# Performance work log

Measured on AMD Instinct MI355X. Metric: run time of the kernel, lower is better.

Reference implementation:

```python
import jax, jax.numpy as jnp
import numpy as np

# config constants
B, T, C = 2, 2048, 1024
N_HEAD = 16
N_FULL = 8           # n_head - int(n_head * ratio_heads)
N_RED = 8            # int(n_head * 0.5)
HEAD_DIM = 64        # C // N_HEAD
RED_DIM = 32         # int(HEAD_DIM * 0.5)
WIN_FULL = 1024      # context_full
WIN_RED = 256        # context_reduced


def setup_inputs() -> dict:
    key = jax.random.key(0)
    ks = jax.random.split(key, 5)
    def w(k, shape, fan_in):
        return jax.random.normal(k, shape, jnp.float32) * (1.0 / np.sqrt(fan_in))
    return {
        "x": jax.random.normal(ks[0], (B, T, C), jnp.float32),
        "w_qkv_full": w(ks[1], (C, 3 * N_FULL * HEAD_DIM), C),
        "w_qk_red": w(ks[2], (C, 2 * N_RED * RED_DIM), C),
        "w_v_red": w(ks[3], (C, N_RED * HEAD_DIM), C),
        "w_proj": w(ks[4], (C, C), C),
    }


def _windowed_attn(q, k, v, window):
    # q,k: [B,H,T,dq], v: [B,H,T,dv]; causal sliding window: 0 <= i-j < window
    d = q.shape[-1]
    scores = jnp.einsum("bhqd,bhkd->bhqk", q, k) / jnp.sqrt(jnp.float32(d))
    i = jnp.arange(q.shape[2])[:, None]
    j = jnp.arange(k.shape[2])[None, :]
    mask = (i - j < 0) | (i - j >= window)
    scores = jnp.where(mask, -jnp.inf, scores)
    p = jax.nn.softmax(scores, axis=-1)
    return jnp.einsum("bhqk,bhkd->bhqd", p, v)


def reference(x, w_qkv_full, w_qk_red, w_v_red, w_proj):
    Bx, Tx, Cx = x.shape
    split_heads = lambda t, d: t.reshape(Bx, Tx, -1, d).transpose(0, 2, 1, 3)

    # full-dim heads
    q, k, v = jnp.split(x @ w_qkv_full, 3, axis=-1)
    y_full = _windowed_attn(split_heads(q, HEAD_DIM), split_heads(k, HEAD_DIM),
                            split_heads(v, HEAD_DIM), WIN_FULL)

    # reduced q/k dim heads (values keep full head_dim)
    qr, kr = jnp.split(x @ w_qk_red, 2, axis=-1)
    vr = x @ w_v_red
    y_red = _windowed_attn(split_heads(qr, RED_DIM), split_heads(kr, RED_DIM),
                           split_heads(vr, HEAD_DIM), WIN_RED)

    y = jnp.concatenate([y_full, y_red], axis=1)          # [B, n_head, T, head_dim]
    y = y.transpose(0, 2, 1, 3).reshape(Bx, Tx, Cx)
    return y @ w_proj
```

## Files before the change

### kernel.cpp

```cpp
#include <hip/hip_runtime.h>
#include <hip/hip_bf16.h>
#include <stdint.h>

#define TT 2048
#define BB 2
#define CC 1024
#define NEGF (-1e30f)

typedef short bf16x8 __attribute__((ext_vector_type(8)));
typedef short bf16x4 __attribute__((ext_vector_type(4)));
typedef float f32x4 __attribute__((ext_vector_type(4)));

__device__ __forceinline__ f32x4 mfma16(bf16x8 a, bf16x8 b, f32x4 c) {
  return __builtin_amdgcn_mfma_f32_16x16x32_bf16(a, b, c, 0, 0, 0);
}

__device__ __forceinline__ uint16_t f2bf(float f) {
  union { float f; uint32_t u; } v; v.f = f;
  uint32_t u = v.u;
  return (uint16_t)((u + 0x7FFFu + ((u >> 16) & 1u)) >> 16);
}

typedef __attribute__((address_space(3))) uint32_t lds_u32;
typedef const __attribute__((address_space(1))) uint32_t glb_u32;
__device__ __forceinline__ void gload_lds16(const uint16_t* g, uint16_t* l) {
  __builtin_amdgcn_global_load_lds((glb_u32*)g, (lds_u32*)l, 16, 0, 0);
}

__global__ __launch_bounds__(256) void k_convert(const float* __restrict__ in,
                                                 uint16_t* __restrict__ out, int n4) {
  int i = blockIdx.x * blockDim.x + threadIdx.x;
  if (i >= n4) return;
  float4 f = ((const float4*)in)[i];
  ushort4 o;
  o.x = f2bf(f.x); o.y = f2bf(f.y); o.z = f2bf(f.z); o.w = f2bf(f.w);
  ((ushort4*)out)[i] = o;
}

__global__ __launch_bounds__(256) void k_transpose(const float* __restrict__ W,
                                                   uint16_t* __restrict__ Wt,
                                                   int K, int N) {
  __shared__ float tile[32][33];
  int tx = threadIdx.x & 31, ty = threadIdx.x >> 5;
  int n0 = blockIdx.x * 32, k0 = blockIdx.y * 32;
#pragma unroll
  for (int r = 0; r < 4; r++)
    tile[ty + r * 8][tx] = W[(size_t)(k0 + ty + r * 8) * N + n0 + tx];
  __syncthreads();
#pragma unroll
  for (int r = 0; r < 4; r++)
    Wt[(size_t)(n0 + ty + r * 8) * K + k0 + tx] = f2bf(tile[tx][ty + r * 8]);
}

template <bool F32OUT>
__global__ __launch_bounds__(256) void k_gemm128(const uint16_t* __restrict__ A,
                                                 const uint16_t* __restrict__ Bt,
                                                 void* __restrict__ Cp,
                                                 int K, int ldc) {
  __shared__ __align__(16) uint16_t Alds[128 * 32];
  __shared__ __align__(16) uint16_t Blds[128 * 32];
  const int tid = threadIdx.x;
  const int lane = tid & 63, wave = tid >> 6;
  const int lr = lane & 15, lg = lane >> 4;
  const int wm = wave & 1, wn = wave >> 1;
  const int m0 = blockIdx.y * 128;
  const int n0 = blockIdx.x * 128;

  f32x4 acc[4][4] = {};

  const int srow = wave * 16 + (lane >> 2);
  const int scol = (lane & 3) * 8;
  const uint16_t* pa_l = A + (size_t)(m0 + srow) * K + scol;
  const uint16_t* pb_l = Bt + (size_t)(n0 + srow) * K + scol;
  uint16_t* alds_w0 = &Alds[(wave * 64) * 8];
  uint16_t* alds_w1 = &Alds[(256 + wave * 64) * 8];
  uint16_t* blds_w0 = &Blds[(wave * 64) * 8];
  uint16_t* blds_w1 = &Blds[(256 + wave * 64) * 8];

  for (int k0 = 0; k0 < K; k0 += 32) {
    __syncthreads();
    gload_lds16(pa_l + k0, alds_w0);
    gload_lds16(pa_l + (size_t)64 * K + k0, alds_w1);
    gload_lds16(pb_l + k0, blds_w0);
    gload_lds16(pb_l + (size_t)64 * K + k0, blds_w1);
    __syncthreads();

    bf16x8 af[4], bfr[4];
#pragma unroll
    for (int mi = 0; mi < 4; mi++)
      af[mi] = *(const bf16x8*)&Alds[(wm * 64 + mi * 16 + lr) * 32 + lg * 8];
#pragma unroll
    for (int ni = 0; ni < 4; ni++)
      bfr[ni] = *(const bf16x8*)&Blds[(wn * 64 + ni * 16 + lr) * 32 + lg * 8];
#pragma unroll
    for (int mi = 0; mi < 4; mi++)
#pragma unroll
      for (int ni = 0; ni < 4; ni++)
        acc[mi][ni] = mfma16(af[mi], bfr[ni], acc[mi][ni]);
  }

#pragma unroll
  for (int mi = 0; mi < 4; mi++)
#pragma unroll
    for (int ni = 0; ni < 4; ni++)
#pragma unroll
      for (int r = 0; r < 4; r++) {
        size_t idx = (size_t)(m0 + wm * 64 + mi * 16 + lg * 4 + r) * ldc
                   + n0 + wn * 64 + ni * 16 + lr;
        if (F32OUT) ((float*)Cp)[idx] = acc[mi][ni][r];
        else        ((uint16_t*)Cp)[idx] = f2bf(acc[mi][ni][r]);
      }
}

__global__ __launch_bounds__(256) void k_vtrans(const uint16_t* __restrict__ QKV,
                                                uint16_t* __restrict__ Vt) {
  __shared__ uint16_t tile[64][72];
  int t0 = blockIdx.x * 64;
  int h = blockIdx.y, b = blockIdx.z;
  int vOff = (h < 8) ? (1024 + h * 64) : (2048 + (h - 8) * 64);
  const uint16_t* src = QKV + ((size_t)b * TT + t0) * 2560 + vOff;
  int tx = threadIdx.x & 15, ty = threadIdx.x >> 4;
#pragma unroll
  for (int p = 0; p < 4; p++)
    *(ushort4*)&tile[ty + p * 16][tx * 4] =
        *(const ushort4*)(src + (size_t)(ty + p * 16) * 2560 + tx * 4);
  __syncthreads();
  uint16_t* dst = Vt + ((size_t)(b * 16 + h) * 64) * TT + t0;
#pragma unroll
  for (int p = 0; p < 4; p++) {
    int dv = ty + p * 16;
    ushort4 o;
    o.x = tile[tx * 4 + 0][dv];
    o.y = tile[tx * 4 + 1][dv];
    o.z = tile[tx * 4 + 2][dv];
    o.w = tile[tx * 4 + 3][dv];
    *(ushort4*)(dst + (size_t)dv * TT + tx * 4) = o;
  }
}

__global__ __launch_bounds__(256) void k_attn(const uint16_t* __restrict__ QKV,
                                              const uint16_t* __restrict__ Vt,
                                              uint16_t* __restrict__ Y) {
  __shared__ __align__(16) uint16_t Klds[64 * 64];
  __shared__ __align__(16) uint16_t Vlds[64 * 64];
  __shared__ __align__(16) uint16_t Plds[4][16][72];
  const int tid = threadIdx.x;
  const int lane = tid & 63, wave = tid >> 6;
  const int lr = lane & 15, lg = lane >> 4;
  const int qt = blockIdx.x & 31;
  const int h = (blockIdx.x >> 5) & 15;
  const int b = blockIdx.x >> 9;
  const int q0b = qt * 64;
  const int q0 = q0b + wave * 16;

  int dqk, window, qOff, kOff;
  if (h < 8) { dqk = 64; window = 1024; qOff = h * 64; kOff = 512 + h * 64; }
  else { int hr = h - 8; dqk = 32; window = 256; qOff = 1536 + hr * 32; kOff = 1792 + hr * 32; }
  const float scale = (dqk == 64) ? 0.125f : 0.17677669529663687f;
  const uint16_t* base = QKV + (size_t)b * TT * 2560;
  const uint16_t* vt = Vt + ((size_t)(b * 16 + h) * 64) * TT;
  const int nf = dqk >> 5;

  bf16x8 qf[2];
  for (int s = 0; s < nf; s++)
    qf[s] = *(const bf16x8*)(base + (size_t)(q0 + lr) * 2560 + qOff + s * 32 + lg * 8);

  float m = NEGF, lsum = 0.f;
  f32x4 o[4] = {};

  int klo_b = q0b - window + 1; if (klo_b < 0) klo_b = 0; klo_b &= ~63;
  const int klo_w = (q0 - window + 1 < 0) ? 0 : (q0 - window + 1);
  const int khi_w = q0 + 15;
  const int q = q0 + lr;

  for (int k0 = klo_b; k0 <= q0b + 63; k0 += 64) {
    __syncthreads();
    if (nf == 2) {
#pragma unroll
      for (int j = 0; j < 2; j++) {
        int c = j * 256 + tid;
        int row = c >> 3, cl = c & 7, sc = cl ^ (row & 7);
        gload_lds16(base + (size_t)(k0 + row) * 2560 + kOff + sc * 8,
                    &Klds[(j * 256 + wave * 64) * 8]);
      }
    } else {
      int row = tid >> 2, cl = tid & 3, sc = cl ^ (row & 3);
      gload_lds16(base + (size_t)(k0 + row) * 2560 + kOff + sc * 8,
                  &Klds[(wave * 64) * 8]);
    }
#pragma unroll
    for (int j = 0; j < 2; j++) {
      int c = j * 256 + tid;
      int row = c >> 3, cl = c & 7, sc = cl ^ (row & 7);
      gload_lds16(vt + (size_t)row * TT + k0 + sc * 8,
                  &Vlds[(j * 256 + wave * 64) * 8]);
    }
    __syncthreads();

    if (k0 > khi_w || k0 + 63 < klo_w) continue;

    f32x4 st[4];
#pragma unroll
    for (int hh = 0; hh < 4; hh++) {
      f32x4 acc = {0.f, 0.f, 0.f, 0.f};
      int row = hh * 16 + lr;
      if (nf == 2) {
        acc = mfma16(*(const bf16x8*)&Klds[row * 64 + ((lg) ^ (row & 7)) * 8], qf[0], acc);
        acc = mfma16(*(const bf16x8*)&Klds[row * 64 + ((4 + lg) ^ (row & 7)) * 8], qf[1], acc);
      } else {
        acc = mfma16(*(const bf16x8*)&Klds[row * 32 + ((lg) ^ (row & 3)) * 8], qf[0], acc);
      }
      st[hh] = acc;
    }
    float tmax = NEGF;
    const bool interior = (k0 + 63 <= q0) && (q0 + 15 - k0 < window);
    if (interior) {
#pragma unroll
      for (int hh = 0; hh < 4; hh++)
#pragma unroll
        for (int r = 0; r < 4; r++) {
          float sv = st[hh][r] * scale;
          st[hh][r] = sv;
          tmax = fmaxf(tmax, sv);
        }
    } else {
#pragma unroll
      for (int hh = 0; hh < 4; hh++)
#pragma unroll
        for (int r = 0; r < 4; r++) {
          int key = k0 + 16 * hh + lg * 4 + r;
          bool ok = (key <= q) && (q - key < window);
          float sv = ok ? st[hh][r] * scale : NEGF;
          st[hh][r] = sv;
          tmax = fmaxf(tmax, sv);
        }
    }
    tmax = fmaxf(tmax, __shfl_xor(tmax, 16));
    tmax = fmaxf(tmax, __shfl_xor(tmax, 32));
    if (!__all(tmax <= m)) {
      float mn = fmaxf(m, tmax);
      float alpha = __expf(m - mn);
      lsum *= alpha;
#pragma unroll
      for (int d = 0; d < 4; d++) o[d] *= alpha;
      m = mn;
    }
    float psum = 0.f;
#pragma unroll
    for (int hh = 0; hh < 4; hh++) {
      bf16x4 pk;
#pragma unroll
      for (int r = 0; r < 4; r++) {
        float sv = st[hh][r];
        float p = (sv > -0.5e30f) ? __expf(sv - m) : 0.f;
        psum += p;
        pk[r] = (short)f2bf(p);
      }
      *(bf16x4*)&Plds[wave][lr][16 * hh + lg * 4] = pk;
    }
    psum += __shfl_xor(psum, 16);
    psum += __shfl_xor(psum, 32);
    lsum += psum;

#pragma unroll
    for (int ks = 0; ks < 2; ks++) {
      bf16x8 pf = *(const bf16x8*)&Plds[wave][lr][ks * 32 + lg * 8];
#pragma unroll
      for (int db = 0; db < 4; db++) {
        int row = db * 16 + lr;
        bf16x8 vf = *(const bf16x8*)&Vlds[row * 64 + ((4 * ks + lg) ^ (row & 7)) * 8];
        o[db] = mfma16(vf, pf, o[db]);
      }
    }
  }
  const float inv = 1.0f / lsum;
  uint16_t* yp = Y + ((size_t)b * TT + q0 + lr) * CC + h * 64;
#pragma unroll
  for (int db = 0; db < 4; db++)
#pragma unroll
    for (int r = 0; r < 4; r++)
      yp[db * 16 + lg * 4 + r] = f2bf(o[db][r] * inv);
}

extern "C" void kernel_launch(void* const* d_in, const int* in_sizes, int n_in,
                              void* d_out, int out_size, void* d_ws, size_t ws_size,
                              hipStream_t stream) {
  const float* x    = (const float*)d_in[0];
  const float* wqkv = (const float*)d_in[1];
  const float* wqk  = (const float*)d_in[2];
  const float* wv   = (const float*)d_in[3];
  const float* wp   = (const float*)d_in[4];

  uint16_t* ws  = (uint16_t*)d_ws;
  uint16_t* xb  = ws;
  uint16_t* WtA = xb  + (size_t)4096 * 1024;
  uint16_t* WtP = WtA + (size_t)2560 * 1024;
  uint16_t* QKV = WtP + (size_t)1024 * 1024;
  uint16_t* Yb  = QKV + (size_t)4096 * 2560;
  uint16_t* Vt  = xb;

  k_convert<<<4096, 256, 0, stream>>>(x, xb, 4096 * 1024 / 4);
  k_transpose<<<dim3(48, 32), 256, 0, stream>>>(wqkv, WtA, 1024, 1536);
  k_transpose<<<dim3(16, 32), 256, 0, stream>>>(wqk, WtA + (size_t)1536 * 1024, 1024, 512);
  k_transpose<<<dim3(16, 32), 256, 0, stream>>>(wv,  WtA + (size_t)2048 * 1024, 1024, 512);
  k_transpose<<<dim3(32, 32), 256, 0, stream>>>(wp,  WtP, 1024, 1024);
  k_gemm128<false><<<dim3(20, 32), 256, 0, stream>>>(xb, WtA, QKV, 1024, 2560);
  k_vtrans<<<dim3(32, 16, 2), 256, 0, stream>>>(QKV, Vt);
  k_attn<<<1024, 256, 0, stream>>>(QKV, Vt, Yb);
  k_gemm128<true><<<dim3(8, 32), 256, 0, stream>>>(Yb, WtP, (float*)d_out, 1024, 1024);
}
```

Measured before the change: 203.9 us.

## Double-buffer K/V LDS tiles in attention to overlap loads with compute

The attention kernel now keeps two LDS buffers for K and V and issues the async global-to-LDS loads for the next key tile before computing on the current one. This replaces the two barriers per iteration with a single vmcnt wait plus barrier at the end. It also raises wave priority around the MFMA sections. The goal is to hide global load latency behind the QK and PV matmuls, at the cost of doubling K/V LDS use, which may lower occupancy.

After: 204.6 us. Within noise of the previous version (+0.4%).

```diff
diff --git a/kernel.cpp b/kernel.cpp
--- a/kernel.cpp
+++ b/kernel.cpp
@@ -141,8 +141,8 @@
 __global__ __launch_bounds__(256) void k_attn(const uint16_t* __restrict__ QKV,
                                               const uint16_t* __restrict__ Vt,
                                               uint16_t* __restrict__ Y) {
-  __shared__ __align__(16) uint16_t Klds[64 * 64];
-  __shared__ __align__(16) uint16_t Vlds[64 * 64];
+  __shared__ __align__(16) uint16_t Klds[2][64 * 64];
+  __shared__ __align__(16) uint16_t Vlds[2][64 * 64];
   __shared__ __align__(16) uint16_t Plds[4][16][72];
   const int tid = threadIdx.x;
   const int lane = tid & 63, wave = tid >> 6;
@@ -172,106 +172,126 @@
   const int klo_w = (q0 - window + 1 < 0) ? 0 : (q0 - window + 1);
   const int khi_w = q0 + 15;
   const int q = q0 + lr;
-
-  for (int k0 = klo_b; k0 <= q0b + 63; k0 += 64) {
-    __syncthreads();
+  const int kend = q0b + 63;
+
+  auto stage = [&](int k0, int buf) {
     if (nf == 2) {
 #pragma unroll
       for (int j = 0; j < 2; j++) {
         int c = j * 256 + tid;
         int row = c >> 3, cl = c & 7, sc = cl ^ (row & 7);
         gload_lds16(base + (size_t)(k0 + row) * 2560 + kOff + sc * 8,
-                    &Klds[(j * 256 + wave * 64) * 8]);
+                    &Klds[buf][(j * 256 + wave * 64) * 8]);
       }
     } else {
       int row = tid >> 2, cl = tid & 3, sc = cl ^ (row & 3);
       gload_lds16(base + (size_t)(k0 + row) * 2560 + kOff + sc * 8,
-                  &Klds[(wave * 64) * 8]);
+                  &Klds[buf][(wave * 64) * 8]);
     }
 #pragma unroll
     for (int j = 0; j < 2; j++) {
       int c = j * 256 + tid;
       int row = c >> 3, cl = c & 7, sc = cl ^ (row & 7);
       gload_lds16(vt + (size_t)row * TT + k0 + sc * 8,
-                  &Vlds[(j * 256 + wave * 64) * 8]);
+                  &Vlds[buf][(j * 256 + wave * 64) * 8]);
     }
-    __syncthreads();
-
-    if (k0 > khi_w || k0 + 63 < klo_w) continue;
-
-    f32x4 st[4];
-#pragma unroll
-    for (int hh = 0; hh < 4; hh++) {
-      f32x4 acc = {0.f, 0.f, 0.f, 0.f};
-      int row = hh * 16 + lr;
-      if (nf == 2) {
-        acc = mfma16(*(const bf16x8*)&Klds[row * 64 + ((lg) ^ (row & 7)) * 8], qf[0], acc);
-        acc = mfma16(*(const bf16x8*)&Klds[row * 64 + ((4 + lg) ^ (row & 7)) * 8], qf[1], acc);
+  };
+
+  stage(klo_b, 0);
+  asm volatile("s_waitcnt vmcnt(0)" ::: "memory");
+  __builtin_amdgcn_s_barrier();
+  __builtin_amdgcn_sched_barrier(0);
+
+  int cur = 0;
+  for (int k0 = klo_b; k0 <= kend; k0 += 64) {
+    const int nxt = k0 + 64;
+    if (nxt <= kend) stage(nxt, cur ^ 1);
+
+    if (!(k0 > khi_w || k0 + 63 < klo_w)) {
+      f32x4 st[4];
+      __builtin_amdgcn_s_setprio(1);
+#pragma unroll
+      for (int hh = 0; hh < 4; hh++) {
+        f32x4 acc = {0.f, 0.f, 0.f, 0.f};
+        int row = hh * 16 + lr;
+        if (nf == 2) {
+          acc = mfma16(*(const bf16x8*)&Klds[cur][row * 64 + ((lg) ^ (row & 7)) * 8], qf[0], acc);
+          acc = mfma16(*(const bf16x8*)&Klds[cur][row * 64 + ((4 + lg) ^ (row & 7)) * 8], qf[1], acc);
+        } else {
+          acc = mfma16(*(const bf16x8*)&Klds[cur][row * 32 + ((lg) ^ (row & 3)) * 8], qf[0], acc);
+        }
+        st[hh] = acc;
+      }
+      __builtin_amdgcn_s_setprio(0);
+      float tmax = NEGF;
+      const bool interior = (k0 + 63 <= q0) && (q0 + 15 - k0 < window);
+      if (interior) {
+#pragma unroll
+        for (int hh = 0; hh < 4; hh++)
+#pragma unroll
+          for (int r = 0; r < 4; r++) {
+            float sv = st[hh][r] * scale;
+            st[hh][r] = sv;
+            tmax = fmaxf(tmax, sv);
+          }
       } else {
-        acc = mfma16(*(const bf16x8*)&Klds[row * 32 + ((lg) ^ (row & 3)) * 8], qf[0], acc);
-      }
-      st[hh] = acc;
+#pragma unroll
+        for (int hh = 0; hh < 4; hh++)
+#pragma unroll
+          for (int r = 0; r < 4; r++) {
+            int key = k0 + 16 * hh + lg * 4 + r;
+            bool ok = (key <= q) && (q - key < window);
+            float sv = ok ? st[hh][r] * scale : NEGF;
+            st[hh][r] = sv;
+            tmax = fmaxf(tmax, sv);
+          }
+      }
+      tmax = fmaxf(tmax, __shfl_xor(tmax, 16));
+      tmax = fmaxf(tmax, __shfl_xor(tmax, 32));
+      if (!__all(tmax <= m)) {
+        float mn = fmaxf(m, tmax);
+        float alpha = __expf(m - mn);
+        lsum *= alpha;
+#pragma unroll
+        for (int d = 0; d < 4; d++) o[d] *= alpha;
+        m = mn;
+      }
+      float psum = 0.f;
+#pragma unroll
+      for (int hh = 0; hh < 4; hh++) {
+        bf16x4 pk;
+#pragma unroll
+        for (int r = 0; r < 4; r++) {
+          float sv = st[hh][r];
+          float p = (sv > -0.5e30f) ? __expf(sv - m) : 0.f;
+          psum += p;
+          pk[r] = (short)f2bf(p);
+        }
+        *(bf16x4*)&Plds[wave][lr][16 * hh + lg * 4] = pk;
+      }
+      psum += __shfl_xor(psum, 16);
+      psum += __shfl_xor(psum, 32);
+      lsum += psum;
+
+      __builtin_amdgcn_s_setprio(1);
+#pragma unroll
+      for (int ks = 0; ks < 2; ks++) {
+        bf16x8 pf = *(const bf16x8*)&Plds[wave][lr][ks * 32 + lg * 8];
+#pragma unroll
+        for (int db = 0; db < 4; db++) {
+          int row = db * 16 + lr;
+          bf16x8 vf = *(const bf16x8*)&Vlds[cur][row * 64 + ((4 * ks + lg) ^ (row & 7)) * 8];
+          o[db] = mfma16(vf, pf, o[db]);
+        }
+      }
+      __builtin_amdgcn_s_setprio(0);
     }
-    float tmax = NEGF;
-    const bool interior = (k0 + 63 <= q0) && (q0 + 15 - k0 < window);
-    if (interior) {
-#pragma unroll
-      for (int hh = 0; hh < 4; hh++)
-#pragma unroll
-        for (int r = 0; r < 4; r++) {
-          float sv = st[hh][r] * scale;
-          st[hh][r] = sv;
-          tmax = fmaxf(tmax, sv);
-        }
-    } else {
-#pragma unroll
-      for (int hh = 0; hh < 4; hh++)
-#pragma unroll
-        for (int r = 0; r < 4; r++) {
-          int key = k0 + 16 * hh + lg * 4 + r;
-          bool ok = (key <= q) && (q - key < window);
-          float sv = ok ? st[hh][r] * scale : NEGF;
-          st[hh][r] = sv;
-          tmax = fmaxf(tmax, sv);
-        }
-    }
-    tmax = fmaxf(tmax, __shfl_xor(tmax, 16));
-    tmax = fmaxf(tmax, __shfl_xor(tmax, 32));
-    if (!__all(tmax <= m)) {
-      float mn = fmaxf(m, tmax);
-      float alpha = __expf(m - mn);
-      lsum *= alpha;
-#pragma unroll
-      for (int d = 0; d < 4; d++) o[d] *= alpha;
-      m = mn;
-    }
-    float psum = 0.f;
-#pragma unroll
-    for (int hh = 0; hh < 4; hh++) {
-      bf16x4 pk;
-#pragma unroll
-      for (int r = 0; r < 4; r++) {
-        float sv = st[hh][r];
-        float p = (sv > -0.5e30f) ? __expf(sv - m) : 0.f;
-        psum += p;
-        pk[r] = (short)f2bf(p);
-      }
-      *(bf16x4*)&Plds[wave][lr][16 * hh + lg * 4] = pk;
-    }
-    psum += __shfl_xor(psum, 16);
-    psum += __shfl_xor(psum, 32);
-    lsum += psum;
-
-#pragma unroll
-    for (int ks = 0; ks < 2; ks++) {
-      bf16x8 pf = *(const bf16x8*)&Plds[wave][lr][ks * 32 + lg * 8];
-#pragma unroll
-      for (int db = 0; db < 4; db++) {
-        int row = db * 16 + lr;
-        bf16x8 vf = *(const bf16x8*)&Vlds[row * 64 + ((4 * ks + lg) ^ (row & 7)) * 8];
-        o[db] = mfma16(vf, pf, o[db]);
-      }
-    }
+
+    asm volatile("s_waitcnt vmcnt(0)" ::: "memory");
+    __builtin_amdgcn_sched_barrier(0);
+    __builtin_amdgcn_s_barrier();
+    __builtin_amdgcn_sched_barrier(0);
+    cur ^= 1;
   }
   const float inv = 1.0f / lsum;
   uint16_t* yp = Y + ((size_t)b * TT + q0 + lr) * CC + h * 64;
```
